# Optimization experiments

Measured on AMD Instinct MI355X. Metric: run time of the kernel, lower is better.

## Reference

```python
import jax, jax.numpy as jnp
import numpy as np

N_NODES = 100000
N_EDGES = 1000000
EMB = 64
HID = 64
N_CLASSES = 1
LEAKY_SLOPE = 0.01  # flax.linen.leaky_relu default


def setup_inputs() -> dict:
    key = jax.random.key(0)
    k1, k2, k3, k4, k5 = jax.random.split(key, 5)
    node_ids = jnp.arange(N_NODES, dtype=jnp.int32)
    senders = jax.random.randint(k1, (N_EDGES,), 0, N_NODES, dtype=jnp.int32)
    receivers = jax.random.randint(k2, (N_EDGES,), 0, N_NODES, dtype=jnp.int32)
    embed_table = jax.random.normal(k3, (N_NODES, EMB), dtype=jnp.float32) * 0.05
    W1 = jax.random.normal(k4, (EMB, HID), dtype=jnp.float32) * (1.0 / np.sqrt(EMB))
    W2 = jax.random.normal(k5, (HID, N_CLASSES), dtype=jnp.float32) * (1.0 / np.sqrt(HID))
    b2 = jnp.zeros((N_CLASSES,), dtype=jnp.float32)
    return {"node_ids": node_ids, "senders": senders, "receivers": receivers,
            "embed_table": embed_table, "W1": W1, "W2": W2, "b2": b2}


def gcn_aggregate(x, senders, receivers, n_nodes, symmetric):
    # Faithful to jraph.GraphConvolution: update_node_fn is applied BEFORE this.
    if symmetric:
        ones = jnp.ones_like(senders, dtype=x.dtype)
        send_deg = jax.ops.segment_sum(ones, senders, num_segments=n_nodes)
        recv_deg = jax.ops.segment_sum(ones, receivers, num_segments=n_nodes)
        x = x * jax.lax.rsqrt(jnp.maximum(send_deg, 1.0))[:, None]
        x = jax.ops.segment_sum(x[senders], receivers, num_segments=n_nodes)  # [N, d]
        x = x * jax.lax.rsqrt(jnp.maximum(recv_deg, 1.0))[:, None]
    else:
        x = jax.ops.segment_sum(x[senders], receivers, num_segments=n_nodes)
    return x


def reference(node_ids, senders, receivers, embed_table, W1, W2, b2):
    n = node_ids.shape[0]
    # GraphMapFeatures(embed_node_fn=nn.Embed(...))
    x = embed_table[node_ids]                      # [N, EMB]
    # GraphConvolution(Dense(hidden, use_bias=False), symmetric_normalization=True)
    x = x @ W1                                     # [N, HID]
    x = gcn_aggregate(x, senders, receivers, n, symmetric=True)
    x = jax.nn.leaky_relu(x, negative_slope=LEAKY_SLOPE)
    # GraphConvolution(Dense(classes), symmetric_normalization=False)
    x = x @ W2 + b2                                # [N, C]
    x = gcn_aggregate(x, senders, receivers, n, symmetric=False)
    return jax.nn.sigmoid(x)
```

## Files before the change

### kernel.cpp

```cpp
#include <hip/hip_runtime.h>
#include <hip/hip_bf16.h>

#define N_NODES 100000
#define N_EDGES 1000000
#define SCAN_B 256
#define N_BLOCKS_RS ((N_NODES + 255) / 256)
#define N_BLOCKS_A  ((N_NODES + 63) / 64)
#define H_BLOCKS 1024

#define CHUNKS 40
#define CHUNK_E 25000
#define HWORDS 25000


__device__ __forceinline__ unsigned f32_to_bf16(float v) {
    unsigned u = __float_as_uint(v);
    return (u + 0x7fffu + ((u >> 16) & 1u)) >> 16;
}

__global__ void k_hist8(const int4* __restrict__ s4,
                        const int4* __restrict__ r4,
                        unsigned* __restrict__ ghist_s8,
                        unsigned* __restrict__ ghist_r8,
                        unsigned char* __restrict__ rank8) {
    __shared__ unsigned lds[HWORDS];
    int b   = blockIdx.x;
    int isR = (b < CHUNKS);
    int c   = isR ? b : b - CHUNKS;
    int t   = threadIdx.x;

    for (int w = t; w < HWORDS; w += 1024) lds[w] = 0u;
    __syncthreads();

    int beg = c * (CHUNK_E / 4);
    int end = beg + CHUNK_E / 4;
    if (isR) {
        for (int q = beg + t; q < end; q += 1024) {
            int4 v = r4[q];
            int sh0 = (v.x & 3) * 8, sh1 = (v.y & 3) * 8;
            int sh2 = (v.z & 3) * 8, sh3 = (v.w & 3) * 8;
            unsigned o0 = atomicAdd(&lds[v.x >> 2], 1u << sh0);
            unsigned o1 = atomicAdd(&lds[v.y >> 2], 1u << sh1);
            unsigned o2 = atomicAdd(&lds[v.z >> 2], 1u << sh2);
            unsigned o3 = atomicAdd(&lds[v.w >> 2], 1u << sh3);
            uchar4 rk;
            rk.x = (unsigned char)((o0 >> sh0) & 0xffu);
            rk.y = (unsigned char)((o1 >> sh1) & 0xffu);
            rk.z = (unsigned char)((o2 >> sh2) & 0xffu);
            rk.w = (unsigned char)((o3 >> sh3) & 0xffu);
            *(uchar4*)(rank8 + 4 * (size_t)q) = rk;
        }
    } else {
        for (int q = beg + t; q < end; q += 1024) {
            int4 v = s4[q];
            atomicAdd(&lds[v.x >> 2], 1u << ((v.x & 3) * 8));
            atomicAdd(&lds[v.y >> 2], 1u << ((v.y & 3) * 8));
            atomicAdd(&lds[v.z >> 2], 1u << ((v.z & 3) * 8));
            atomicAdd(&lds[v.w >> 2], 1u << ((v.w & 3) * 8));
        }
    }
    __syncthreads();

    uint4* __restrict__ dst =
        (uint4*)((isR ? ghist_r8 : ghist_s8) + (size_t)c * HWORDS);
    const uint4* lsrc = (const uint4*)lds;
    for (int w = t; w < HWORDS / 4; w += 1024) dst[w] = lsrc[w];
}

__global__ void k_scanA(const unsigned char* __restrict__ gs8,
                        const unsigned char* __restrict__ gr8,
                        unsigned char* __restrict__ base8,
                        int* __restrict__ part,
                        float* __restrict__ rs,
                        int* __restrict__ blockSums) {
    __shared__ int s[64];
    int t = threadIdx.x;
    int g = t >> 2, sl = t & 3;
    int node = blockIdx.x * 64 + g;
    int total = 0;
    if (node < N_NODES) {
        unsigned ss = 0;
#pragma unroll
        for (int k = 0; k < 10; ++k)
            ss += gs8[(size_t)(sl * 10 + k) * N_NODES + node];
        ss += __shfl_xor(ss, 1, 64);
        ss += __shfl_xor(ss, 2, 64);
        if (sl == 0) rs[node] = rsqrtf(fmaxf((float)ss, 1.0f));

        unsigned rv[10];
        unsigned rsum = 0;
#pragma unroll
        for (int k = 0; k < 10; ++k) {
            rv[k] = gr8[(size_t)(sl * 10 + k) * N_NODES + node];
            rsum += rv[k];
        }
        unsigned x = rsum;
        unsigned u1 = __shfl_up(x, 1, 4); if (sl >= 1) x += u1;
        unsigned u2 = __shfl_up(x, 2, 4); if (sl >= 2) x += u2;
        unsigned run = x - rsum;
        total = (int)__shfl(x, 3, 4);
#pragma unroll
        for (int k = 0; k < 10; ++k) {
            base8[(size_t)(sl * 10 + k) * N_NODES + node] = (unsigned char)run;
            run += rv[k];
        }
    }
    if (sl == 0) s[g] = total;
    __syncthreads();
    if (t < 64) {
        int v = s[t];
        int acc = v;
#pragma unroll
        for (int off = 1; off < 64; off <<= 1) {
            int y = __shfl_up(acc, off, 64);
            if (t >= off) acc += y;
        }
        s[t] = acc - v;
        if (t == 63) blockSums[blockIdx.x] = acc;
    }
    __syncthreads();
    if (sl == 0 && node < N_NODES) part[node] = s[g];
}

__global__ void k_scanCD_h(const int* __restrict__ part,
                           const int* __restrict__ blockSums,
                           int* __restrict__ row_start,
                           const float* __restrict__ emb,
                           const float* __restrict__ rs,
                           const float* __restrict__ W1,
                           unsigned short* __restrict__ h16) {
    __shared__ int s[SCAN_B];
    __shared__ int gsum[4];
    int t = threadIdx.x;
    int b = blockIdx.x;

    if (b < N_BLOCKS_RS) {
        int acc = 0;
        for (int j = t; j < 4 * b; j += SCAN_B) acc += blockSums[j];
        s[t] = acc;
        __syncthreads();
        for (int off = SCAN_B / 2; off > 0; off >>= 1) {
            if (t < off) s[t] += s[t + off];
            __syncthreads();
        }
        int blockOff = s[0];
        if (t < 4)
            gsum[t] = (4 * b + t < N_BLOCKS_A) ? blockSums[4 * b + t] : 0;
        __syncthreads();

        int gi = t >> 6;
        int goff = blockOff;
        if (gi > 0) goff += gsum[0];
        if (gi > 1) goff += gsum[1];
        if (gi > 2) goff += gsum[2];
        int n = b * SCAN_B + t;
        if (n < N_NODES) row_start[n] = goff + part[n];
        if (b == 0 && t == 0) row_start[N_NODES] = N_EDGES;
    } else {
        int lane = t & 63;
        int wib  = t >> 6;
        int gw   = (b - N_BLOCKS_RS) * 4 + wib;
        const int nw = H_BLOCKS * 4;

        float w1c[64];
#pragma unroll
        for (int k = 0; k < 64; ++k) w1c[k] = W1[k * 64 + lane];

        for (int n = gw; n < N_NODES; n += nw) {
            float e = emb[(size_t)n * 64 + lane] * rs[n];
            float a0 = 0.f, a1 = 0.f, a2 = 0.f, a3 = 0.f;
            int ei = __float_as_int(e);
#pragma unroll
            for (int k = 0; k < 16; ++k) {
                a0 += __int_as_float(__builtin_amdgcn_readlane(ei, 4 * k + 0)) * w1c[4 * k + 0];
                a1 += __int_as_float(__builtin_amdgcn_readlane(ei, 4 * k + 1)) * w1c[4 * k + 1];
                a2 += __int_as_float(__builtin_amdgcn_readlane(ei, 4 * k + 2)) * w1c[4 * k + 2];
                a3 += __int_as_float(__builtin_amdgcn_readlane(ei, 4 * k + 3)) * w1c[4 * k + 3];
            }
            float a = (a0 + a1) + (a2 + a3);
            h16[(size_t)n * 64 + lane] = (unsigned short)f32_to_bf16(a);
        }
    }
}

__global__ void k_fill(const int4* __restrict__ s4,
                       const int4* __restrict__ r4,
                       const uchar4* __restrict__ rk4,
                       const unsigned char* __restrict__ base8,
                       const int* __restrict__ row_start,
                       int* __restrict__ col) {
    int i = blockIdx.x * blockDim.x + threadIdx.x;
    if (i >= N_EDGES / 4) return;
    int c = (4 * i) / CHUNK_E;
    const unsigned char* __restrict__ bs = base8 + (size_t)c * N_NODES;
    int4 s = s4[i];
    int4 r = r4[i];
    uchar4 rk = rk4[i];
    col[row_start[r.x] + bs[r.x] + rk.x] = s.x;
    col[row_start[r.y] + bs[r.y] + rk.y] = s.y;
    col[row_start[r.z] + bs[r.z] + rk.z] = s.z;
    col[row_start[r.w] + bs[r.w] + rk.w] = s.w;
}

__global__ void k_agg_post(const int* __restrict__ row_start,
                           const int* __restrict__ col,
                           const uint4* __restrict__ h128,
                           const float* __restrict__ W2,
                           const float* __restrict__ b2,
                           float* __restrict__ z) {
    int wid  = (blockIdx.x * blockDim.x + threadIdx.x) >> 6;
    int lane = threadIdx.x & 63;
    if (wid >= N_NODES) return;
    int eslot = lane >> 3;
    int fq    = lane & 7;

    int start = row_start[wid];
    int end   = row_start[wid + 1];
    float a0 = 0.f, a1 = 0.f, a2 = 0.f, a3 = 0.f;
    float a4 = 0.f, a5 = 0.f, a6 = 0.f, a7 = 0.f;
    for (int i = start + eslot; i < end; i += 8) {
        int sx = col[i];
        uint4 u = h128[(size_t)sx * 8 + fq];
        a0 += __uint_as_float(u.x << 16);
        a1 += __uint_as_float(u.x & 0xffff0000u);
        a2 += __uint_as_float(u.y << 16);
        a3 += __uint_as_float(u.y & 0xffff0000u);
        a4 += __uint_as_float(u.z << 16);
        a5 += __uint_as_float(u.z & 0xffff0000u);
        a6 += __uint_as_float(u.w << 16);
        a7 += __uint_as_float(u.w & 0xffff0000u);
    }
#pragma unroll
    for (int off = 8; off < 64; off <<= 1) {
        a0 += __shfl_xor(a0, off, 64);
        a1 += __shfl_xor(a1, off, 64);
        a2 += __shfl_xor(a2, off, 64);
        a3 += __shfl_xor(a3, off, 64);
        a4 += __shfl_xor(a4, off, 64);
        a5 += __shfl_xor(a5, off, 64);
        a6 += __shfl_xor(a6, off, 64);
        a7 += __shfl_xor(a7, off, 64);
    }
    float rsq = rsqrtf(fmaxf((float)(end - start), 1.0f));
    float4 wA = ((const float4*)W2)[fq * 2];
    float4 wB = ((const float4*)W2)[fq * 2 + 1];
    float p = 0.f, x;
    x = a0 * rsq; x = (x > 0.f) ? x : 0.01f * x; p += x * wA.x;
    x = a1 * rsq; x = (x > 0.f) ? x : 0.01f * x; p += x * wA.y;
    x = a2 * rsq; x = (x > 0.f) ? x : 0.01f * x; p += x * wA.z;
    x = a3 * rsq; x = (x > 0.f) ? x : 0.01f * x; p += x * wA.w;
    x = a4 * rsq; x = (x > 0.f) ? x : 0.01f * x; p += x * wB.x;
    x = a5 * rsq; x = (x > 0.f) ? x : 0.01f * x; p += x * wB.y;
    x = a6 * rsq; x = (x > 0.f) ? x : 0.01f * x; p += x * wB.z;
    x = a7 * rsq; x = (x > 0.f) ? x : 0.01f * x; p += x * wB.w;
    p += __shfl_xor(p, 1, 64);
    p += __shfl_xor(p, 2, 64);
    p += __shfl_xor(p, 4, 64);
    if (lane == 0) z[wid] = p + b2[0];
}

__global__ void k_agg2_sigmoid(const int* __restrict__ row_start,
                               const int* __restrict__ col,
                               const float* __restrict__ z,
                               float* __restrict__ out) {
    int gtid = blockIdx.x * blockDim.x + threadIdx.x;
    int n  = gtid >> 2;
    int sl = gtid & 3;
    if (n >= N_NODES) return;
    int start = row_start[n];
    int end   = row_start[n + 1];
    float acc = 0.f;
    for (int i = start + sl; i < end; i += 4) acc += z[col[i]];
    acc += __shfl_xor(acc, 1, 64);
    acc += __shfl_xor(acc, 2, 64);
    if (sl == 0) out[n] = 1.0f / (1.0f + expf(-acc));
}

extern "C" void kernel_launch(void* const* d_in, const int* in_sizes, int n_in,
                              void* d_out, int out_size, void* d_ws, size_t ws_size,
                              hipStream_t stream) {
    const int* senders    = (const int*)d_in[1];
    const int* receivers  = (const int*)d_in[2];
    const float* emb      = (const float*)d_in[3];
    const float* W1       = (const float*)d_in[4];
    const float* W2       = (const float*)d_in[5];
    const float* b2       = (const float*)d_in[6];
    float* out            = (float*)d_out;

    char* ws = (char*)d_ws;
    unsigned char*  ghist_s8  = (unsigned char*)(ws);
    unsigned char*  ghist_r8  = (unsigned char*)(ws + 4000000);
    unsigned char*  base8     = (unsigned char*)(ws + 8000000);
    unsigned char*  rank8     = (unsigned char*)(ws + 12000000);
    int*            part      = (int*)(ws + 13000000);
    int*            row_start = (int*)(ws + 13400000);
    int*            blockSums = (int*)(ws + 13800016);
    float*          rs        = (float*)(ws + 13807600);
    int*            col       = (int*)(ws + 14207600);
    unsigned short* h16       = (unsigned short*)(ws + 18207616);
    float*          z         = (float*)(ws + 31007616);

    const int B = 256;
    const int QBLK = (N_EDGES / 4 + B - 1) / B;

    k_hist8<<<2 * CHUNKS, 1024, 0, stream>>>(
        (const int4*)senders, (const int4*)receivers,
        (unsigned*)ghist_s8, (unsigned*)ghist_r8, rank8);
    k_scanA<<<N_BLOCKS_A, B, 0, stream>>>(
        ghist_s8, ghist_r8, base8, part, rs, blockSums);
    k_scanCD_h<<<N_BLOCKS_RS + H_BLOCKS, B, 0, stream>>>(
        part, blockSums, row_start, emb, rs, W1, h16);
    k_fill<<<QBLK, B, 0, stream>>>(
        (const int4*)senders, (const int4*)receivers,
        (const uchar4*)rank8, base8, row_start, col);
    k_agg_post<<<(N_NODES * 64) / B, B, 0, stream>>>(
        row_start, col, (const uint4*)h16, W2, b2, z);
    k_agg2_sigmoid<<<(N_NODES * 4 + B - 1) / B, B, 0, stream>>>(
        row_start, col, z, out);
}
```

Before: 184.3 us.

## Overlap node MLP with histogram kernel by moving sender-degree scaling into aggregation

```diff
diff --git a/kernel.cpp b/kernel.cpp
--- a/kernel.cpp
+++ b/kernel.cpp
@@ -6,11 +6,13 @@
 #define SCAN_B 256
 #define N_BLOCKS_RS ((N_NODES + 255) / 256)
 #define N_BLOCKS_A  ((N_NODES + 63) / 64)
-#define H_BLOCKS 1024
 
 #define CHUNKS 40
 #define CHUNK_E 25000
 #define HWORDS 25000
+#define HIST_BLOCKS (2 * CHUNKS)
+#define MLP_BLOCKS 176
+#define MLP_WAVES (MLP_BLOCKS * 16)
 
 
 __device__ __forceinline__ unsigned f32_to_bf16(float v) {
@@ -18,16 +20,44 @@
     return (u + 0x7fffu + ((u >> 16) & 1u)) >> 16;
 }
 
-__global__ void k_hist8(const int4* __restrict__ s4,
-                        const int4* __restrict__ r4,
-                        unsigned* __restrict__ ghist_s8,
-                        unsigned* __restrict__ ghist_r8,
-                        unsigned char* __restrict__ rank8) {
+__global__ void k_hist8_mlp(const int4* __restrict__ s4,
+                            const int4* __restrict__ r4,
+                            unsigned* __restrict__ ghist_s8,
+                            unsigned* __restrict__ ghist_r8,
+                            unsigned char* __restrict__ rank8,
+                            const float* __restrict__ emb,
+                            const float* __restrict__ W1,
+                            unsigned short* __restrict__ h16) {
     __shared__ unsigned lds[HWORDS];
-    int b   = blockIdx.x;
+    int b = blockIdx.x;
+    int t = threadIdx.x;
+
+    if (b >= HIST_BLOCKS) {
+        int lane = t & 63;
+        int gw   = (b - HIST_BLOCKS) * 16 + (t >> 6);
+        float w1c[64];
+#pragma unroll
+        for (int k = 0; k < 64; ++k) w1c[k] = W1[k * 64 + lane];
+
+        for (int n = gw; n < N_NODES; n += MLP_WAVES) {
+            float e = emb[(size_t)n * 64 + lane];
+            float a0 = 0.f, a1 = 0.f, a2 = 0.f, a3 = 0.f;
+            int ei = __float_as_int(e);
+#pragma unroll
+            for (int k = 0; k < 16; ++k) {
+                a0 += __int_as_float(__builtin_amdgcn_readlane(ei, 4 * k + 0)) * w1c[4 * k + 0];
+                a1 += __int_as_float(__builtin_amdgcn_readlane(ei, 4 * k + 1)) * w1c[4 * k + 1];
+                a2 += __int_as_float(__builtin_amdgcn_readlane(ei, 4 * k + 2)) * w1c[4 * k + 2];
+                a3 += __int_as_float(__builtin_amdgcn_readlane(ei, 4 * k + 3)) * w1c[4 * k + 3];
+            }
+            float a = (a0 + a1) + (a2 + a3);
+            h16[(size_t)n * 64 + lane] = (unsigned short)f32_to_bf16(a);
+        }
+        return;
+    }
+
     int isR = (b < CHUNKS);
     int c   = isR ? b : b - CHUNKS;
-    int t   = threadIdx.x;
 
     for (int w = t; w < HWORDS; w += 1024) lds[w] = 0u;
     __syncthreads();
@@ -122,65 +152,35 @@
     if (sl == 0 && node < N_NODES) part[node] = s[g];
 }
 
-__global__ void k_scanCD_h(const int* __restrict__ part,
-                           const int* __restrict__ blockSums,
-                           int* __restrict__ row_start,
-                           const float* __restrict__ emb,
-                           const float* __restrict__ rs,
-                           const float* __restrict__ W1,
-                           unsigned short* __restrict__ h16) {
+__global__ void k_rows(const int* __restrict__ part,
+                       const int* __restrict__ blockSums,
+                       int* __restrict__ row_start) {
     __shared__ int s[SCAN_B];
     __shared__ int gsum[4];
     int t = threadIdx.x;
     int b = blockIdx.x;
 
-    if (b < N_BLOCKS_RS) {
-        int acc = 0;
-        for (int j = t; j < 4 * b; j += SCAN_B) acc += blockSums[j];
-        s[t] = acc;
+    int acc = 0;
+    for (int j = t; j < 4 * b; j += SCAN_B) acc += blockSums[j];
+    s[t] = acc;
+    __syncthreads();
+    for (int off = SCAN_B / 2; off > 0; off >>= 1) {
+        if (t < off) s[t] += s[t + off];
         __syncthreads();
-        for (int off = SCAN_B / 2; off > 0; off >>= 1) {
-            if (t < off) s[t] += s[t + off];
-            __syncthreads();
-        }
-        int blockOff = s[0];
-        if (t < 4)
-            gsum[t] = (4 * b + t < N_BLOCKS_A) ? blockSums[4 * b + t] : 0;
-        __syncthreads();
-
-        int gi = t >> 6;
-        int goff = blockOff;
-        if (gi > 0) goff += gsum[0];
-        if (gi > 1) goff += gsum[1];
-        if (gi > 2) goff += gsum[2];
-        int n = b * SCAN_B + t;
-        if (n < N_NODES) row_start[n] = goff + part[n];
-        if (b == 0 && t == 0) row_start[N_NODES] = N_EDGES;
-    } else {
-        int lane = t & 63;
-        int wib  = t >> 6;
-        int gw   = (b - N_BLOCKS_RS) * 4 + wib;
-        const int nw = H_BLOCKS * 4;
-
-        float w1c[64];
-#pragma unroll
-        for (int k = 0; k < 64; ++k) w1c[k] = W1[k * 64 + lane];
-
-        for (int n = gw; n < N_NODES; n += nw) {
-            float e = emb[(size_t)n * 64 + lane] * rs[n];
-            float a0 = 0.f, a1 = 0.f, a2 = 0.f, a3 = 0.f;
-            int ei = __float_as_int(e);
-#pragma unroll
-            for (int k = 0; k < 16; ++k) {
-                a0 += __int_as_float(__builtin_amdgcn_readlane(ei, 4 * k + 0)) * w1c[4 * k + 0];
-                a1 += __int_as_float(__builtin_amdgcn_readlane(ei, 4 * k + 1)) * w1c[4 * k + 1];
-                a2 += __int_as_float(__builtin_amdgcn_readlane(ei, 4 * k + 2)) * w1c[4 * k + 2];
-                a3 += __int_as_float(__builtin_amdgcn_readlane(ei, 4 * k + 3)) * w1c[4 * k + 3];
-            }
-            float a = (a0 + a1) + (a2 + a3);
-            h16[(size_t)n * 64 + lane] = (unsigned short)f32_to_bf16(a);
-        }
-    }
+    }
+    int blockOff = s[0];
+    if (t < 4)
+        gsum[t] = (4 * b + t < N_BLOCKS_A) ? blockSums[4 * b + t] : 0;
+    __syncthreads();
+
+    int gi = t >> 6;
+    int goff = blockOff;
+    if (gi > 0) goff += gsum[0];
+    if (gi > 1) goff += gsum[1];
+    if (gi > 2) goff += gsum[2];
+    int n = b * SCAN_B + t;
+    if (n < N_NODES) row_start[n] = goff + part[n];
+    if (b == 0 && t == 0) row_start[N_NODES] = N_EDGES;
 }
 
 __global__ void k_fill(const int4* __restrict__ s4,
@@ -205,6 +205,7 @@
 __global__ void k_agg_post(const int* __restrict__ row_start,
                            const int* __restrict__ col,
                            const uint4* __restrict__ h128,
+                           const float* __restrict__ rs,
                            const float* __restrict__ W2,
                            const float* __restrict__ b2,
                            float* __restrict__ z) {
@@ -220,15 +221,16 @@
     float a4 = 0.f, a5 = 0.f, a6 = 0.f, a7 = 0.f;
     for (int i = start + eslot; i < end; i += 8) {
         int sx = col[i];
+        float rss = rs[sx];
         uint4 u = h128[(size_t)sx * 8 + fq];
-        a0 += __uint_as_float(u.x << 16);
-        a1 += __uint_as_float(u.x & 0xffff0000u);
-        a2 += __uint_as_float(u.y << 16);
-        a3 += __uint_as_float(u.y & 0xffff0000u);
-        a4 += __uint_as_float(u.z << 16);
-        a5 += __uint_as_float(u.z & 0xffff0000u);
-        a6 += __uint_as_float(u.w << 16);
-        a7 += __uint_as_float(u.w & 0xffff0000u);
+        a0 += rss * __uint_as_float(u.x << 16);
+        a1 += rss * __uint_as_float(u.x & 0xffff0000u);
+        a2 += rss * __uint_as_float(u.y << 16);
+        a3 += rss * __uint_as_float(u.y & 0xffff0000u);
+        a4 += rss * __uint_as_float(u.z << 16);
+        a5 += rss * __uint_as_float(u.z & 0xffff0000u);
+        a6 += rss * __uint_as_float(u.w << 16);
+        a7 += rss * __uint_as_float(u.w & 0xffff0000u);
     }
 #pragma unroll
     for (int off = 8; off < 64; off <<= 1) {
@@ -303,18 +305,17 @@
     const int B = 256;
     const int QBLK = (N_EDGES / 4 + B - 1) / B;
 
-    k_hist8<<<2 * CHUNKS, 1024, 0, stream>>>(
+    k_hist8_mlp<<<HIST_BLOCKS + MLP_BLOCKS, 1024, 0, stream>>>(
         (const int4*)senders, (const int4*)receivers,
-        (unsigned*)ghist_s8, (unsigned*)ghist_r8, rank8);
+        (unsigned*)ghist_s8, (unsigned*)ghist_r8, rank8, emb, W1, h16);
     k_scanA<<<N_BLOCKS_A, B, 0, stream>>>(
         ghist_s8, ghist_r8, base8, part, rs, blockSums);
-    k_scanCD_h<<<N_BLOCKS_RS + H_BLOCKS, B, 0, stream>>>(
-        part, blockSums, row_start, emb, rs, W1, h16);
+    k_rows<<<N_BLOCKS_RS, SCAN_B, 0, stream>>>(part, blockSums, row_start);
     k_fill<<<QBLK, B, 0, stream>>>(
         (const int4*)senders, (const int4*)receivers,
         (const uchar4*)rank8, base8, row_start, col);
     k_agg_post<<<(N_NODES * 64) / B, B, 0, stream>>>(
-        row_start, col, (const uint4*)h16, W2, b2, z);
+        row_start, col, (const uint4*)h16, rs, W2, b2, z);
     k_agg2_sigmoid<<<(N_NODES * 4 + B - 1) / B, B, 0, stream>>>(
         row_start, col, z, out);
 }
```

Result: slower. 190.1 us (+3.1%).
